# Optimization experiments

Measured on AMD Instinct MI355X. Metric: run time of the kernel, lower is better.

The kernel has to match this reference:

```python
import jax, jax.numpy as jnp
import numpy as np

N_NODES = 50000
N_EDGES = 800000
F_IN = 128
HIDDEN = 128
N_CLASSES = 10
N_GRAPHS = 256


def _glorot(key, shape):
    lim = float(np.sqrt(6.0 / (shape[0] + shape[1])))
    return jax.random.uniform(key, shape, jnp.float32, -lim, lim)


def setup_inputs() -> dict:
    key = jax.random.key(0)
    ks = jax.random.split(key, 12)
    x = jax.random.normal(ks[0], (N_NODES, F_IN), jnp.float32)
    edge_index = jax.random.randint(ks[1], (2, N_EDGES), 0, N_NODES, jnp.int64)
    batch = jnp.sort(jax.random.randint(ks[2], (N_NODES,), 0, N_GRAPHS, jnp.int64))
    dims = [(F_IN, HIDDEN), (HIDDEN, HIDDEN), (HIDDEN, N_CLASSES)]
    params = {}
    for i, (din, dout) in enumerate(dims, start=1):
        params[f"Wl{i}"] = _glorot(ks[2 + 2 * i], (din, dout))   # lin_l: applied to aggregated neighbors (has bias)
        params[f"bl{i}"] = jnp.zeros((dout,), jnp.float32)
        params[f"Wr{i}"] = _glorot(ks[3 + 2 * i], (din, dout))   # lin_r: applied to root/self features (no bias)
    return {"x": x, "edge_index": edge_index, "batch": batch, **params}


def _sage_conv(x, src, dst, Wl, bl, Wr):
    # mean aggregation of source features at destination nodes
    msg = x[src]                                                    # [E, D] gather
    ssum = jax.ops.segment_sum(msg, dst, num_segments=N_NODES)      # [N, D]
    cnt = jax.ops.segment_sum(jnp.ones((src.shape[0],), x.dtype), dst, num_segments=N_NODES)
    agg = ssum / jnp.maximum(cnt, 1.0)[:, None]
    return agg @ Wl + bl + x @ Wr


def reference(x, edge_index, batch, Wl1, bl1, Wr1, Wl2, bl2, Wr2, Wl3, bl3, Wr3):
    src, dst = edge_index[0], edge_index[1]
    h = _sage_conv(x, src, dst, Wl1, bl1, Wr1)
    h = _sage_conv(h, src, dst, Wl2, bl2, Wr2)
    h = _sage_conv(h, src, dst, Wl3, bl3, Wr3)                      # [N, C]
    # global mean pool over graphs
    gsum = jax.ops.segment_sum(h, batch, num_segments=N_GRAPHS)     # [G, C]
    gcnt = jax.ops.segment_sum(jnp.ones((h.shape[0],), h.dtype), batch, num_segments=N_GRAPHS)
    pooled = gsum / jnp.maximum(gcnt, 1.0)[:, None]
    return jax.nn.log_softmax(pooled, axis=-1)
```

## Files before the change

kernel.cpp:

```cpp
#include <hip/hip_runtime.h>


#define CAP 48
#define EB 4096

typedef __attribute__((ext_vector_type(8))) short short8;
typedef __attribute__((ext_vector_type(4))) float floatx4;

static __device__ __forceinline__ unsigned short f2bf(float f) {
    unsigned int u = __float_as_uint(f);
    u += 0x7FFFu + ((u >> 16) & 1u);
    return (unsigned short)(u >> 16);
}
static __device__ __forceinline__ float bf2f(unsigned short b) {
    return __uint_as_float(((unsigned int)b) << 16);
}
static __device__ __forceinline__ unsigned int packbf2(float a, float b) {
    return (unsigned int)f2bf(a) | ((unsigned int)f2bf(b) << 16);
}

__global__ void prep0(int* __restrict__ cnt, int N,
                      int* __restrict__ zero_base, int zero_words,
                      unsigned int* __restrict__ y3z, unsigned int* __restrict__ u1z,
                      unsigned int* __restrict__ u2w) {
    int idx = blockIdx.x * 256 + threadIdx.x;
    if (idx < N) { cnt[idx] = 0; return; }
    idx -= N;
    if (idx < zero_words) { zero_base[idx] = 0; return; }
    idx -= zero_words;
    if (idx < 6)  { y3z[(size_t)N * 6 + idx] = 0; return; }
    if (idx < 12) { u1z[(size_t)N * 6 + (idx - 6)] = 0; return; }
    if (idx < 18) { u2w[(size_t)N * 6 + (idx - 12)] = 0; return; }
}

__global__ void prep1(const int* __restrict__ ei, int E, int ablk, int N,
                      int* __restrict__ cnt, unsigned short* __restrict__ colbuf,
                      const float* __restrict__ Wl2, const float* __restrict__ Wr2,
                      const float* __restrict__ Wl3, const float* __restrict__ Wr3,
                      float* __restrict__ m2Mg) {
    __shared__ float wtT_s[128 * 20];
    if (blockIdx.x < (unsigned)ablk) {
        int e0 = blockIdx.x * EB + threadIdx.x;
#pragma unroll
        for (int k = 0; k < 16; ++k) {
            int e = e0 + k * 256;
            if (e < E) {
                int src = ei[e];
                int dst = ei[E + e];
                int slot = atomicAdd(&cnt[dst], 1);
                if (slot < CAP)
                    colbuf[(size_t)dst * CAP + slot] = (unsigned short)src;
            }
        }
        return;
    }
    int rb = blockIdx.x - ablk;
    const int tid = threadIdx.x;
    for (int i = tid; i < 2560; i += 256) {
        int f = i / 20, c = i - f * 20;
        wtT_s[i] = (c < 10) ? Wl3[f * 10 + c] : Wr3[f * 10 + (c - 10)];
    }
    __syncthreads();
    int jl = tid >> 3;
    int cg = tid & 7;
    int j = rb * 32 + jl;
    const float* w2row = ((cg < 4) ? Wl2 : Wr2) + (size_t)j * 128;
    int c20 = (cg & 3) * 5;
    float acc[5] = {0.f, 0.f, 0.f, 0.f, 0.f};
    for (int f4 = 0; f4 < 32; ++f4) {
        float4 wv = *(const float4*)&w2row[f4 * 4];
#pragma unroll
        for (int e = 0; e < 4; ++e) {
            float w = (e == 0) ? wv.x : (e == 1) ? wv.y : (e == 2) ? wv.z : wv.w;
            const float* wt = &wtT_s[(f4 * 4 + e) * 20 + c20];
#pragma unroll
            for (int i = 0; i < 5; ++i) acc[i] += w * wt[i];
        }
    }
    int cc = (cg >> 2) * 20 + c20;
#pragma unroll
    for (int i = 0; i < 5; ++i) m2Mg[j * 40 + cc + i] = acc[i];
}

__global__ __launch_bounds__(256) void prep2(
    const float* __restrict__ Wl1, const float* __restrict__ Wr1,
    const float* __restrict__ Wl3, const float* __restrict__ Wr3,
    const float* __restrict__ bl1, const float* __restrict__ bl2,
    const float* __restrict__ bl3,
    const float* __restrict__ m2Mg, short* __restrict__ Wq,
    float* __restrict__ cbv) {
    __shared__ float m2s[128 * 40];
    __shared__ float aLR[32][80];
    const int tid = threadIdx.x;
    if (blockIdx.x == 4) {
        for (int i = tid; i < 3072; i += 256) {
            int k = i & 127;
            int t = i >> 7;
            int mt = t / 6, m = 10 + t % 6;
            int ks = k >> 5, rem = k & 31, qq = rem >> 3, jj = rem & 7;
            int l = qq * 16 + m;
            Wq[(((mt * 4 + ks) * 64) + l) * 8 + jj] = 0;
        }
        if (tid < 30) {
            float s = 0.f;
            if (tid < 10) {
                int c = tid;
                for (int k = 0; k < 128; ++k) s += bl1[k] * m2Mg[k * 40 + c];
            } else if (tid < 20) {
                int c = tid - 10;
                for (int k = 0; k < 128; ++k)
                    s += bl1[k] * (m2Mg[k * 40 + 20 + c] + m2Mg[k * 40 + 10 + c]);
                for (int f = 0; f < 128; ++f) s += bl2[f] * Wl3[f * 10 + c];
            } else {
                int c = tid - 20;
                for (int k = 0; k < 128; ++k) s += bl1[k] * m2Mg[k * 40 + 30 + c];
                for (int f = 0; f < 128; ++f) s += bl2[f] * Wr3[f * 10 + c];
                s += bl3[c];
            }
            cbv[tid] = s;
        }
        return;
    }
    for (int i = tid; i < 5120; i += 256) m2s[i] = m2Mg[i];
    __syncthreads();
    int kl = tid >> 3;
    int cg = tid & 7;
    int k = blockIdx.x * 32 + kl;
    int c0 = cg * 5;
    const float* wl = Wl1 + (size_t)k * 128;
    const float* wr = Wr1 + (size_t)k * 128;
    float accL[5] = {0.f, 0.f, 0.f, 0.f, 0.f};
    float accR[5] = {0.f, 0.f, 0.f, 0.f, 0.f};
    for (int j4 = 0; j4 < 32; ++j4) {
        float4 wa = *(const float4*)&wl[j4 * 4];
        float4 wb = *(const float4*)&wr[j4 * 4];
#pragma unroll
        for (int e = 0; e < 4; ++e) {
            float wle = (e == 0) ? wa.x : (e == 1) ? wa.y : (e == 2) ? wa.z : wa.w;
            float wre = (e == 0) ? wb.x : (e == 1) ? wb.y : (e == 2) ? wb.z : wb.w;
            const float* mr = &m2s[(j4 * 4 + e) * 40 + c0];
#pragma unroll
            for (int i = 0; i < 5; ++i) {
                accL[i] += wle * mr[i];
                accR[i] += wre * mr[i];
            }
        }
    }
#pragma unroll
    for (int i = 0; i < 5; ++i) {
        aLR[kl][c0 + i] = accL[i];
        aLR[kl][40 + c0 + i] = accR[i];
    }
    __syncthreads();
    int ks = k >> 5, rem = k & 31, qq = rem >> 3, jj = rem & 7;
#pragma unroll
    for (int i = 0; i < 5; ++i) {
        int f = c0 + i;
        float val;
        if (f < 10) {
            val = aLR[kl][f];
        } else if (f < 20) {
            int c = f - 10;
            val = aLR[kl][40 + c] + aLR[kl][20 + c] + aLR[kl][10 + c];
        } else if (f < 30) {
            int c = f - 20;
            val = aLR[kl][40 + 10 + c] + aLR[kl][40 + 20 + c] + aLR[kl][30 + c];
        } else {
            int c = f - 30;
            val = aLR[kl][40 + 30 + c];
        }
        int mt = f / 10, c = f % 10;
        int l = qq * 16 + c;
        Wq[(((mt * 4 + ks) * 64) + l) * 8 + jj] = (short)f2bf(val);
    }
}

__global__ __launch_bounds__(256) void fillX(
    const float* __restrict__ x, const short* __restrict__ Wq,
    unsigned short* __restrict__ y3, float* __restrict__ yS, int N) {
    __shared__ unsigned short As[64 * 136];
    int node0 = blockIdx.x * 64;
#pragma unroll
    for (int c = 0; c < 8; ++c) {
        int idx = c * 256 + threadIdx.x;
        int r = idx >> 5;
        int c4 = idx & 31;
        int row = node0 + r;
        float4 v = make_float4(0.f, 0.f, 0.f, 0.f);
        if (row < N) v = *(const float4*)&x[(size_t)row * 128 + c4 * 4];
        ushort4 p;
        p.x = f2bf(v.x); p.y = f2bf(v.y); p.z = f2bf(v.z); p.w = f2bf(v.w);
        *(ushort4*)&As[r * 136 + c4 * 4] = p;
    }
    __syncthreads();

    const int w = threadIdx.x >> 6;
    const int lane = threadIdx.x & 63;
    const int q = lane >> 4;
    const int m = lane & 15;

    floatx4 acc[4] = {};
#pragma unroll
    for (int s = 0; s < 4; ++s) {
        short8 bfrag = *(const short8*)&As[(w * 16 + m) * 136 + s * 32 + q * 8];
#pragma unroll
        for (int mi = 0; mi < 4; ++mi) {
            short8 wf = *(const short8*)&Wq[((mi * 4 + s) * 64 + lane) * 8];
            acc[mi] = __builtin_amdgcn_mfma_f32_16x16x32_bf16(
                wf, bfrag, acc[mi], 0, 0, 0);
        }
    }
    int node = node0 + w * 16 + m;
    if (node < N) {
        int l = q * 4;
        {
            floatx4 a = acc[0];
            if (l < 8) {
                ushort4 p;
                p.x = f2bf(a[0]); p.y = f2bf(a[1]);
                p.z = f2bf(a[2]); p.w = f2bf(a[3]);
                *(ushort4*)&y3[(size_t)node * 12 + l] = p;
            } else if (l == 8) {
                ushort2 p2;
                p2.x = f2bf(a[0]); p2.y = f2bf(a[1]);
                *(ushort2*)&y3[(size_t)node * 12 + 8] = p2;
            }
        }
#pragma unroll
        for (int mi = 1; mi < 4; ++mi) {
            floatx4 a = acc[mi];
            size_t off = (size_t)node * 36 + (mi - 1) * 12 + l;
            if (l < 8) {
                *(float4*)&yS[off] = make_float4(a[0], a[1], a[2], a[3]);
            } else if (l == 8) {
                *(float2*)&yS[off] = make_float2(a[0], a[1]);
            }
        }
    }
}

__global__ __launch_bounds__(256) void g1(
    const unsigned int* __restrict__ y3z, const int* __restrict__ cnt,
    const unsigned short* __restrict__ colbuf, const float2* __restrict__ yS2,
    unsigned int* __restrict__ u1z, int N) {
    const int lane = threadIdx.x & 63;
    const int wvi = threadIdx.x >> 6;
    const int la = lane & 15;
    const int qb = lane & 48;
    const int node = blockIdx.x * 16 + wvi * 4 + (lane >> 4);
    const bool valid = node < N;
    const int nodec = valid ? node : N - 1;
    const int deg = cnt[nodec];
    const int d = valid ? min(deg, CAP) : 0;
    const unsigned short* cb = colbuf + (size_t)nodec * CAP;
    const int sub = (la < 5) ? la : la - 5;

    float f0 = 0.f, f1 = 0.f;
    int nb = (d + 15) >> 4;
    for (int b = 0; b < nb; ++b) {
        int slot = b * 16 + la;
        int idx = (slot < d) ? (int)cb[slot] : N;
        unsigned int vv[8];
#pragma unroll
        for (int j = 0; j < 8; ++j) {
            int s0 = __shfl(idx, qb + 2 * j, 64);
            int s1 = __shfl(idx, qb + 2 * j + 1, 64);
            int sr = (la < 5) ? s0 : s1;
            vv[j] = (la < 10) ? y3z[(size_t)sr * 6 + sub] : 0u;
        }
#pragma unroll
        for (int j = 0; j < 8; ++j) {
            f0 += bf2f((unsigned short)(vv[j] & 0xFFFF));
            f1 += bf2f((unsigned short)(vv[j] >> 16));
        }
    }
    int pl = (la < 5) ? (lane + 5) : (lane - 5);
    f0 += __shfl(f0, pl, 64);
    f1 += __shfl(f1, pl, 64);
    if (valid && la < 5) {
        float inv = 1.0f / (float)max(deg, 1);
        float2 sv = yS2[(size_t)node * 18 + la];
        u1z[(size_t)node * 6 + la] = packbf2(f0 * inv + sv.x, f1 * inv + sv.y);
    }
}

__global__ __launch_bounds__(256) void g2(
    const unsigned int* __restrict__ u1z, const int* __restrict__ cnt,
    const unsigned short* __restrict__ colbuf, const float2* __restrict__ yS2,
    const float2* __restrict__ cbv2, unsigned int* __restrict__ u2w, int N) {
    const int lane = threadIdx.x & 63;
    const int wvi = threadIdx.x >> 6;
    const int la = lane & 15;
    const int qb = lane & 48;
    const int node = blockIdx.x * 16 + wvi * 4 + (lane >> 4);
    const bool valid = node < N;
    const int nodec = valid ? node : N - 1;
    const int deg = cnt[nodec];
    const int d = valid ? min(deg, CAP) : 0;
    const unsigned short* cb = colbuf + (size_t)nodec * CAP;
    const int sub = (la < 5) ? la : la - 5;

    float f0 = 0.f, f1 = 0.f;
    int nb = (d + 15) >> 4;
    for (int b = 0; b < nb; ++b) {
        int slot = b * 16 + la;
        int idx = (slot < d) ? (int)cb[slot] : N;
        unsigned int vv[8];
#pragma unroll
        for (int j = 0; j < 8; ++j) {
            int s0 = __shfl(idx, qb + 2 * j, 64);
            int s1 = __shfl(idx, qb + 2 * j + 1, 64);
            int sr = (la < 5) ? s0 : s1;
            vv[j] = (la < 10) ? u1z[(size_t)sr * 6 + sub] : 0u;
        }
#pragma unroll
        for (int j = 0; j < 8; ++j) {
            f0 += bf2f((unsigned short)(vv[j] & 0xFFFF));
            f1 += bf2f((unsigned short)(vv[j] >> 16));
        }
    }
    int pl = (la < 5) ? (lane + 5) : (lane - 5);
    f0 += __shfl(f0, pl, 64);
    f1 += __shfl(f1, pl, 64);
    if (valid && la < 5) {
        float inv = 1.0f / (float)max(deg, 1);
        float2 sv = yS2[(size_t)node * 18 + 6 + la];
        float2 v1 = cbv2[la];
        float b0 = sv.x + ((deg > 0) ? v1.x : 0.f);
        float b1 = sv.y + ((deg > 0) ? v1.y : 0.f);
        u2w[(size_t)node * 6 + la] = packbf2(f0 * inv + b0, f1 * inv + b1);
    }
}

__global__ __launch_bounds__(256) void g3pool(
    const unsigned int* __restrict__ u2w, const int* __restrict__ cnt,
    const unsigned short* __restrict__ colbuf, const float2* __restrict__ yS2,
    const float2* __restrict__ cbv2, const int* __restrict__ batch,
    float* __restrict__ gsum, float* __restrict__ gcnt, int N) {
    __shared__ float ls[2816];
    for (int i = threadIdx.x; i < 2816; i += 256) ls[i] = 0.f;
    __syncthreads();

    const int lane = threadIdx.x & 63;
    const int wvi = threadIdx.x >> 6;
    const int la = lane & 15;
    const int qb = lane & 48;
    const int node = blockIdx.x * 16 + wvi * 4 + (lane >> 4);
    const bool valid = node < N;
    const int nodec = valid ? node : N - 1;
    const int deg = cnt[nodec];
    const int d = valid ? min(deg, CAP) : 0;
    const unsigned short* cb = colbuf + (size_t)nodec * CAP;
    const int sub = (la < 5) ? la : la - 5;

    float f0 = 0.f, f1 = 0.f;
    int nb = (d + 15) >> 4;
    for (int b = 0; b < nb; ++b) {
        int slot = b * 16 + la;
        int idx = (slot < d) ? (int)cb[slot] : N;
        unsigned int vv[8];
#pragma unroll
        for (int j = 0; j < 8; ++j) {
            int s0 = __shfl(idx, qb + 2 * j, 64);
            int s1 = __shfl(idx, qb + 2 * j + 1, 64);
            int sr = (la < 5) ? s0 : s1;
            vv[j] = (la < 10) ? u2w[(size_t)sr * 6 + sub] : 0u;
        }
#pragma unroll
        for (int j = 0; j < 8; ++j) {
            f0 += bf2f((unsigned short)(vv[j] & 0xFFFF));
            f1 += bf2f((unsigned short)(vv[j] >> 16));
        }
    }
    int pl = (la < 5) ? (lane + 5) : (lane - 5);
    f0 += __shfl(f0, pl, 64);
    f1 += __shfl(f1, pl, 64);
    if (valid && la < 5) {
        float inv = 1.0f / (float)max(deg, 1);
        float2 y0 = yS2[(size_t)node * 18 + 12 + la];
        float2 v0 = cbv2[5 + la];
        float2 vc = cbv2[10 + la];
        float h0 = f0 * inv + y0.x + ((deg > 0) ? v0.x : 0.f) + vc.x;
        float h1 = f1 * inv + y0.y + ((deg > 0) ? v0.y : 0.f) + vc.y;
        int g = batch[node];
        atomicAdd(&ls[g * 10 + 2 * la], h0);
        atomicAdd(&ls[g * 10 + 2 * la + 1], h1);
        if (la == 0) atomicAdd(&ls[2560 + g], 1.0f);
    }
    __syncthreads();
    for (int i = threadIdx.x; i < 2816; i += 256) {
        float v = ls[i];
        if (v != 0.f) {
            if (i < 2560) atomicAdd(&gsum[i], v);
            else          atomicAdd(&gcnt[i - 2560], v);
        }
    }
}

__global__ void finalize_pool(const float* __restrict__ gsum,
                              const float* __restrict__ gcnt,
                              float* __restrict__ out, int G) {
    int g = blockIdx.x * blockDim.x + threadIdx.x;
    if (g >= G) return;
    float inv = 1.0f / fmaxf(gcnt[g], 1.0f);
    float p[10];
    float m = -1e30f;
#pragma unroll
    for (int c = 0; c < 10; ++c) { p[c] = gsum[g * 10 + c] * inv; m = fmaxf(m, p[c]); }
    float s = 0.f;
#pragma unroll
    for (int c = 0; c < 10; ++c) s += expf(p[c] - m);
    float lse = logf(s);
#pragma unroll
    for (int c = 0; c < 10; ++c) out[g * 10 + c] = p[c] - m - lse;
}

extern "C" void kernel_launch(void* const* d_in, const int* in_sizes, int n_in,
                              void* d_out, int out_size, void* d_ws, size_t ws_size,
                              hipStream_t stream) {
    const float* x    = (const float*)d_in[0];
    const int*   ei   = (const int*)d_in[1];
    const int*   batch= (const int*)d_in[2];
    const float* Wl1  = (const float*)d_in[3];
    const float* bl1  = (const float*)d_in[4];
    const float* Wr1  = (const float*)d_in[5];
    const float* Wl2  = (const float*)d_in[6];
    const float* bl2  = (const float*)d_in[7];
    const float* Wr2  = (const float*)d_in[8];
    const float* Wl3  = (const float*)d_in[9];
    const float* bl3  = (const float*)d_in[10];
    const float* Wr3  = (const float*)d_in[11];
    float* out = (float*)d_out;

    const int N = in_sizes[2];
    const int E = in_sizes[1] / 2;
    const int G = out_size / 10;
    const int ablk = (E + EB - 1) / EB;

    char* ws = (char*)d_ws;
    size_t o = 0;
    float* gsum   = (float*)(ws + o); o += (size_t)G * 10 * 4;
    float* gcnt   = (float*)(ws + o); o += (size_t)G * 4;
    size_t zero_bytes = (o + 255) & ~(size_t)255;
    o = zero_bytes;
    int*            cnt    = (int*)(ws + o);            o += (size_t)N * 4;
    unsigned short* colbuf = (unsigned short*)(ws + o); o += ((size_t)N * CAP * 2 + 255) & ~(size_t)255;
    short*          Wq     = (short*)(ws + o);          o += (size_t)8192 * 2;
    float*          cbv    = (float*)(ws + o);          o += 32 * 4;
    o = (o + 255) & ~(size_t)255;
    float*          m2Mg   = (float*)(ws + o);          o += (size_t)128 * 40 * 4;
    o = (o + 255) & ~(size_t)255;
    unsigned short* y3t    = (unsigned short*)(ws + o); o += (size_t)(N + 1) * 12 * 2;
    o = (o + 255) & ~(size_t)255;
    float*          yS     = (float*)(ws + o);          o += (size_t)N * 36 * 4;
    unsigned short* u1z    = (unsigned short*)(ws + o); o += (size_t)(N + 1) * 12 * 2;
    o = (o + 255) & ~(size_t)255;
    unsigned short* u2w    = (unsigned short*)(ws + o); o += (size_t)(N + 1) * 12 * 2;
    o = (o + 255) & ~(size_t)255;

    int zero_words = (int)(zero_bytes / 4);
    int tot0 = N + zero_words + 18;
    prep0<<<(tot0 + 255) / 256, 256, 0, stream>>>(
        cnt, N, (int*)ws, zero_words,
        (unsigned int*)y3t, (unsigned int*)u1z, (unsigned int*)u2w);

    prep1<<<ablk + 4, 256, 0, stream>>>(ei, E, ablk, N, cnt, colbuf,
                                        Wl2, Wr2, Wl3, Wr3, m2Mg);

    prep2<<<5, 256, 0, stream>>>(Wl1, Wr1, Wl3, Wr3, bl1, bl2, bl3,
                                 m2Mg, Wq, cbv);

    int gblocks = (N + 63) / 64;
    int ablocks = (N + 15) / 16;
    fillX<<<gblocks, 256, 0, stream>>>(x, Wq, y3t, yS, N);

    g1<<<ablocks, 256, 0, stream>>>((const unsigned int*)y3t, cnt, colbuf,
                                    (const float2*)yS, (unsigned int*)u1z, N);
    g2<<<ablocks, 256, 0, stream>>>((const unsigned int*)u1z, cnt, colbuf,
                                    (const float2*)yS, (const float2*)cbv,
                                    (unsigned int*)u2w, N);
    g3pool<<<ablocks, 256, 0, stream>>>((const unsigned int*)u2w, cnt, colbuf,
                                        (const float2*)yS, (const float2*)cbv,
                                        batch, gsum, gcnt, N);
    finalize_pool<<<1, 256, 0, stream>>>(gsum, gcnt, out, G);
}
```

Before: 198.4 us.

## Replace global-atomic CSR build with two-pass bucketed edge binning in shared memory

Result: faster. 170.0 us (-14.3%).

```diff
diff --git a/kernel.cpp b/kernel.cpp
--- a/kernel.cpp
+++ b/kernel.cpp
@@ -19,67 +19,81 @@
     return (unsigned int)f2bf(a) | ((unsigned int)f2bf(b) << 16);
 }
 
-__global__ void prep0(int* __restrict__ cnt, int N,
+__global__ void prep1(const int* __restrict__ ei, int E, int ablk, int nbk, int N,
+                      unsigned int* __restrict__ bedges, int* __restrict__ runCnt,
+                      const float* __restrict__ Wl2, const float* __restrict__ Wr2,
+                      const float* __restrict__ Wl3, const float* __restrict__ Wr3,
+                      float* __restrict__ m2Mg,
                       int* __restrict__ zero_base, int zero_words,
                       unsigned int* __restrict__ y3z, unsigned int* __restrict__ u1z,
                       unsigned int* __restrict__ u2w) {
-    int idx = blockIdx.x * 256 + threadIdx.x;
-    if (idx < N) { cnt[idx] = 0; return; }
-    idx -= N;
-    if (idx < zero_words) { zero_base[idx] = 0; return; }
-    idx -= zero_words;
-    if (idx < 6)  { y3z[(size_t)N * 6 + idx] = 0; return; }
-    if (idx < 12) { u1z[(size_t)N * 6 + (idx - 6)] = 0; return; }
-    if (idx < 18) { u2w[(size_t)N * 6 + (idx - 12)] = 0; return; }
-}
-
-__global__ void prep1(const int* __restrict__ ei, int E, int ablk, int N,
-                      int* __restrict__ cnt, unsigned short* __restrict__ colbuf,
-                      const float* __restrict__ Wl2, const float* __restrict__ Wr2,
-                      const float* __restrict__ Wl3, const float* __restrict__ Wr3,
-                      float* __restrict__ m2Mg) {
+    __shared__ int hist[512];
     __shared__ float wtT_s[128 * 20];
     if (blockIdx.x < (unsigned)ablk) {
+        for (int i = threadIdx.x; i < nbk; i += 256) hist[i] = 0;
+        __syncthreads();
         int e0 = blockIdx.x * EB + threadIdx.x;
+        unsigned int pk[16];
+        int bk[16], loc[16];
 #pragma unroll
         for (int k = 0; k < 16; ++k) {
             int e = e0 + k * 256;
             if (e < E) {
                 int src = ei[e];
                 int dst = ei[E + e];
-                int slot = atomicAdd(&cnt[dst], 1);
-                if (slot < CAP)
-                    colbuf[(size_t)dst * CAP + slot] = (unsigned short)src;
-            }
-        }
+                bk[k] = dst >> 7;
+                pk[k] = ((unsigned int)(dst & 127) << 16) | (unsigned int)src;
+                loc[k] = atomicAdd(&hist[bk[k]], 1);
+            } else bk[k] = -1;
+        }
+        __syncthreads();
+        for (int i = threadIdx.x; i < nbk; i += 256)
+            runCnt[(size_t)blockIdx.x * nbk + i] = hist[i];
+#pragma unroll
+        for (int k = 0; k < 16; ++k)
+            if (bk[k] >= 0 && loc[k] < CAP)
+                bedges[((size_t)bk[k] * ablk + blockIdx.x) * CAP + loc[k]] = pk[k];
         return;
     }
     int rb = blockIdx.x - ablk;
-    const int tid = threadIdx.x;
-    for (int i = tid; i < 2560; i += 256) {
-        int f = i / 20, c = i - f * 20;
-        wtT_s[i] = (c < 10) ? Wl3[f * 10 + c] : Wr3[f * 10 + (c - 10)];
-    }
-    __syncthreads();
-    int jl = tid >> 3;
-    int cg = tid & 7;
-    int j = rb * 32 + jl;
-    const float* w2row = ((cg < 4) ? Wl2 : Wr2) + (size_t)j * 128;
-    int c20 = (cg & 3) * 5;
-    float acc[5] = {0.f, 0.f, 0.f, 0.f, 0.f};
-    for (int f4 = 0; f4 < 32; ++f4) {
-        float4 wv = *(const float4*)&w2row[f4 * 4];
-#pragma unroll
-        for (int e = 0; e < 4; ++e) {
-            float w = (e == 0) ? wv.x : (e == 1) ? wv.y : (e == 2) ? wv.z : wv.w;
-            const float* wt = &wtT_s[(f4 * 4 + e) * 20 + c20];
-#pragma unroll
-            for (int i = 0; i < 5; ++i) acc[i] += w * wt[i];
-        }
-    }
-    int cc = (cg >> 2) * 20 + c20;
-#pragma unroll
-    for (int i = 0; i < 5; ++i) m2Mg[j * 40 + cc + i] = acc[i];
+    if (rb < 4) {
+        const int tid = threadIdx.x;
+        for (int i = tid; i < 2560; i += 256) {
+            int f = i / 20, c = i - f * 20;
+            wtT_s[i] = (c < 10) ? Wl3[f * 10 + c] : Wr3[f * 10 + (c - 10)];
+        }
+        __syncthreads();
+        int jl = tid >> 3;
+        int cg = tid & 7;
+        int j = rb * 32 + jl;
+        const float* w2row = ((cg < 4) ? Wl2 : Wr2) + (size_t)j * 128;
+        int c20 = (cg & 3) * 5;
+        float acc[5] = {0.f, 0.f, 0.f, 0.f, 0.f};
+        for (int f4 = 0; f4 < 32; ++f4) {
+            float4 wv = *(const float4*)&w2row[f4 * 4];
+#pragma unroll
+            for (int e = 0; e < 4; ++e) {
+                float w = (e == 0) ? wv.x : (e == 1) ? wv.y : (e == 2) ? wv.z : wv.w;
+                const float* wt = &wtT_s[(f4 * 4 + e) * 20 + c20];
+#pragma unroll
+                for (int i = 0; i < 5; ++i) acc[i] += w * wt[i];
+            }
+        }
+        int cc = (cg >> 2) * 20 + c20;
+#pragma unroll
+        for (int i = 0; i < 5; ++i) m2Mg[j * 40 + cc + i] = acc[i];
+        return;
+    }
+    if (rb == 4) {
+        if (threadIdx.x < 6)  y3z[(size_t)N * 6 + threadIdx.x] = 0;
+        if (threadIdx.x >= 32 && threadIdx.x < 38)
+            u1z[(size_t)N * 6 + (threadIdx.x - 32)] = 0;
+        if (threadIdx.x >= 64 && threadIdx.x < 70)
+            u2w[(size_t)N * 6 + (threadIdx.x - 64)] = 0;
+        return;
+    }
+    int i = (rb - 5) * 256 + threadIdx.x;
+    if (i < zero_words) zero_base[i] = 0;
 }
 
 __global__ __launch_bounds__(256) void prep2(
@@ -177,65 +191,92 @@
 
 __global__ __launch_bounds__(256) void fillX(
     const float* __restrict__ x, const short* __restrict__ Wq,
-    unsigned short* __restrict__ y3, float* __restrict__ yS, int N) {
+    unsigned short* __restrict__ y3, float* __restrict__ yS, int N,
+    int nbk, int ablk,
+    const unsigned int* __restrict__ bedges, const int* __restrict__ runCnt,
+    int* __restrict__ cnt, unsigned short* __restrict__ colbuf) {
     __shared__ unsigned short As[64 * 136];
-    int node0 = blockIdx.x * 64;
-#pragma unroll
-    for (int c = 0; c < 8; ++c) {
-        int idx = c * 256 + threadIdx.x;
-        int r = idx >> 5;
-        int c4 = idx & 31;
-        int row = node0 + r;
-        float4 v = make_float4(0.f, 0.f, 0.f, 0.f);
-        if (row < N) v = *(const float4*)&x[(size_t)row * 128 + c4 * 4];
-        ushort4 p;
-        p.x = f2bf(v.x); p.y = f2bf(v.y); p.z = f2bf(v.z); p.w = f2bf(v.w);
-        *(ushort4*)&As[r * 136 + c4 * 4] = p;
-    }
-    __syncthreads();
-
-    const int w = threadIdx.x >> 6;
-    const int lane = threadIdx.x & 63;
-    const int q = lane >> 4;
-    const int m = lane & 15;
-
-    floatx4 acc[4] = {};
-#pragma unroll
-    for (int s = 0; s < 4; ++s) {
-        short8 bfrag = *(const short8*)&As[(w * 16 + m) * 136 + s * 32 + q * 8];
-#pragma unroll
-        for (int mi = 0; mi < 4; ++mi) {
-            short8 wf = *(const short8*)&Wq[((mi * 4 + s) * 64 + lane) * 8];
-            acc[mi] = __builtin_amdgcn_mfma_f32_16x16x32_bf16(
-                wf, bfrag, acc[mi], 0, 0, 0);
-        }
-    }
-    int node = node0 + w * 16 + m;
-    if (node < N) {
-        int l = q * 4;
-        {
-            floatx4 a = acc[0];
-            if (l < 8) {
-                ushort4 p;
-                p.x = f2bf(a[0]); p.y = f2bf(a[1]);
-                p.z = f2bf(a[2]); p.w = f2bf(a[3]);
-                *(ushort4*)&y3[(size_t)node * 12 + l] = p;
-            } else if (l == 8) {
-                ushort2 p2;
-                p2.x = f2bf(a[0]); p2.y = f2bf(a[1]);
-                *(ushort2*)&y3[(size_t)node * 12 + 8] = p2;
-            }
-        }
-#pragma unroll
-        for (int mi = 1; mi < 4; ++mi) {
-            floatx4 a = acc[mi];
-            size_t off = (size_t)node * 36 + (mi - 1) * 12 + l;
-            if (l < 8) {
-                *(float4*)&yS[off] = make_float4(a[0], a[1], a[2], a[3]);
-            } else if (l == 8) {
-                *(float2*)&yS[off] = make_float2(a[0], a[1]);
-            }
-        }
+    __shared__ int lcnt[128];
+    if (blockIdx.x >= (unsigned)nbk) {
+        int blk = blockIdx.x - nbk;
+        int node0 = blk * 64;
+#pragma unroll
+        for (int c = 0; c < 8; ++c) {
+            int idx = c * 256 + threadIdx.x;
+            int r = idx >> 5;
+            int c4 = idx & 31;
+            int row = node0 + r;
+            float4 v = make_float4(0.f, 0.f, 0.f, 0.f);
+            if (row < N) v = *(const float4*)&x[(size_t)row * 128 + c4 * 4];
+            ushort4 p;
+            p.x = f2bf(v.x); p.y = f2bf(v.y); p.z = f2bf(v.z); p.w = f2bf(v.w);
+            *(ushort4*)&As[r * 136 + c4 * 4] = p;
+        }
+        __syncthreads();
+
+        const int w = threadIdx.x >> 6;
+        const int lane = threadIdx.x & 63;
+        const int q = lane >> 4;
+        const int m = lane & 15;
+
+        floatx4 acc[4] = {};
+#pragma unroll
+        for (int s = 0; s < 4; ++s) {
+            short8 bfrag = *(const short8*)&As[(w * 16 + m) * 136 + s * 32 + q * 8];
+#pragma unroll
+            for (int mi = 0; mi < 4; ++mi) {
+                short8 wf = *(const short8*)&Wq[((mi * 4 + s) * 64 + lane) * 8];
+                acc[mi] = __builtin_amdgcn_mfma_f32_16x16x32_bf16(
+                    wf, bfrag, acc[mi], 0, 0, 0);
+            }
+        }
+        int node = node0 + w * 16 + m;
+        if (node < N) {
+            int l = q * 4;
+            {
+                floatx4 a = acc[0];
+                if (l < 8) {
+                    ushort4 p;
+                    p.x = f2bf(a[0]); p.y = f2bf(a[1]);
+                    p.z = f2bf(a[2]); p.w = f2bf(a[3]);
+                    *(ushort4*)&y3[(size_t)node * 12 + l] = p;
+                } else if (l == 8) {
+                    ushort2 p2;
+                    p2.x = f2bf(a[0]); p2.y = f2bf(a[1]);
+                    *(ushort2*)&y3[(size_t)node * 12 + 8] = p2;
+                }
+            }
+#pragma unroll
+            for (int mi = 1; mi < 4; ++mi) {
+                floatx4 a = acc[mi];
+                size_t off = (size_t)node * 36 + (mi - 1) * 12 + l;
+                if (l < 8) {
+                    *(float4*)&yS[off] = make_float4(a[0], a[1], a[2], a[3]);
+                } else if (l == 8) {
+                    *(float2*)&yS[off] = make_float2(a[0], a[1]);
+                }
+            }
+        }
+    } else {
+        int b = blockIdx.x;
+        if (threadIdx.x < 128) lcnt[threadIdx.x] = 0;
+        __syncthreads();
+        for (int blk = threadIdx.x; blk < ablk; blk += 256) {
+            int c = runCnt[(size_t)blk * nbk + b];
+            c = min(c, CAP);
+            size_t ebase = ((size_t)b * ablk + blk) * CAP;
+            for (int i = 0; i < c; ++i) {
+                unsigned int pk = bedges[ebase + i];
+                int dl = pk >> 16;
+                int slot = atomicAdd(&lcnt[dl], 1);
+                if (slot < CAP)
+                    colbuf[(size_t)(b * 128 + dl) * CAP + slot] =
+                        (unsigned short)(pk & 0xFFFFu);
+            }
+        }
+        __syncthreads();
+        int node = b * 128 + threadIdx.x;
+        if (threadIdx.x < 128 && node < N) cnt[node] = lcnt[threadIdx.x];
     }
 }
 
@@ -436,6 +477,7 @@
     const int E = in_sizes[1] / 2;
     const int G = out_size / 10;
     const int ablk = (E + EB - 1) / EB;
+    const int nbk  = (N + 127) >> 7;
 
     char* ws = (char*)d_ws;
     size_t o = 0;
@@ -457,22 +499,25 @@
     o = (o + 255) & ~(size_t)255;
     unsigned short* u2w    = (unsigned short*)(ws + o); o += (size_t)(N + 1) * 12 * 2;
     o = (o + 255) & ~(size_t)255;
+    unsigned int*   bedges = (unsigned int*)(ws + o);   o += (size_t)nbk * ablk * CAP * 4;
+    int*            runCnt = (int*)(ws + o);            o += (size_t)ablk * nbk * 4;
 
     int zero_words = (int)(zero_bytes / 4);
-    int tot0 = N + zero_words + 18;
-    prep0<<<(tot0 + 255) / 256, 256, 0, stream>>>(
-        cnt, N, (int*)ws, zero_words,
+    int zblocks = (zero_words + 255) / 256;
+    prep1<<<ablk + 5 + zblocks, 256, 0, stream>>>(
+        ei, E, ablk, nbk, N, bedges, runCnt,
+        Wl2, Wr2, Wl3, Wr3, m2Mg,
+        (int*)ws, zero_words,
         (unsigned int*)y3t, (unsigned int*)u1z, (unsigned int*)u2w);
-
-    prep1<<<ablk + 4, 256, 0, stream>>>(ei, E, ablk, N, cnt, colbuf,
-                                        Wl2, Wr2, Wl3, Wr3, m2Mg);
 
     prep2<<<5, 256, 0, stream>>>(Wl1, Wr1, Wl3, Wr3, bl1, bl2, bl3,
                                  m2Mg, Wq, cbv);
 
     int gblocks = (N + 63) / 64;
     int ablocks = (N + 15) / 16;
-    fillX<<<gblocks, 256, 0, stream>>>(x, Wq, y3t, yS, N);
+    fillX<<<nbk + gblocks, 256, 0, stream>>>(x, Wq, y3t, yS, N,
+                                             nbk, ablk, bedges, runCnt,
+                                             cnt, colbuf);
 
     g1<<<ablocks, 256, 0, stream>>>((const unsigned int*)y3t, cnt, colbuf,
                                     (const float2*)yS, (unsigned int*)u1z, N);
```
